# Performance work log

Hardware: AMD Instinct MI355X
Metric: run time of the kernel (lower is better)

## Reference

```python
import jax, jax.numpy as jnp
import numpy as np
from jax import lax

# Model hyperparameters (match init_kwargs)
DIM = 512
N_HEADS = 8
HEAD_DIM = DIM // N_HEADS
N_LAYERS = 4
N_LEVELS = 3          # len(chunk_sizes); CMS forward = stack of MLPs per level
HIDDEN = 4 * DIM
VOCAB = 50257
MAX_SEQ = 2048
B, S = 1, 2048
LN_EPS = 1e-5


def layer_norm(x, w, b):
    m = x.mean(-1, keepdims=True)
    v = ((x - m) ** 2).mean(-1, keepdims=True)
    return (x - m) * lax.rsqrt(v + LN_EPS) * w + b


def linear_attention(x, wq, wk, wv, wo):
    """LinearAttentionWithMemory: fast-weight recurrence M += k v^T, ksum += k,
    y_t = (M_t q_t) / (ksum_t . q_t + 1e-6). x: (B,S,DIM). Weights stored (in,out)."""
    Bn, Sn, D = x.shape
    fmap = lambda z: jax.nn.elu(z) + 1.0  # elu(x)+1 feature map
    # (B,S,D) -> (S,B,H,d) for scan over time
    def proj(w):
        return fmap(x @ w).reshape(Bn, Sn, N_HEADS, HEAD_DIM).transpose(1, 0, 2, 3)
    q = proj(wq)
    k = proj(wk)
    v = fmap(x @ wv).reshape(Bn, Sn, N_HEADS, HEAD_DIM).transpose(1, 0, 2, 3)
    # NOTE: original applies feature_map only to Q and K; V is raw projection
    v = (x @ wv).reshape(Bn, Sn, N_HEADS, HEAD_DIM).transpose(1, 0, 2, 3)

    def step(carry, inp):
        M, ksum = carry            # M: (B,H,d,d), ksum: (B,H,d)
        q_t, k_t, v_t = inp        # each (B,H,d)
        M = M + k_t[..., :, None] * v_t[..., None, :]
        ksum = ksum + k_t
        num = jnp.einsum('bhde,bhd->bhe', M, q_t)
        den = jnp.einsum('bhd,bhd->bh', ksum, q_t)[..., None] + 1e-6
        return (M, ksum), num / den

    carry0 = (jnp.zeros((Bn, N_HEADS, HEAD_DIM, HEAD_DIM), x.dtype),
              jnp.zeros((Bn, N_HEADS, HEAD_DIM), x.dtype))
    _, ys = lax.scan(step, carry0, (q, k, v))          # ys: (S,B,H,d)
    out = ys.transpose(1, 0, 2, 3).reshape(Bn, Sn, D)
    return out @ wo


def cms(x, w1, b1, w2, b2):
    """Continuum Memory System forward: sequential chain of per-level MLPs
    (chunk sizes only control parameter-update frequency during training).
    w1: (N_LEVELS, DIM, HIDDEN), w2: (N_LEVELS, HIDDEN, DIM)."""
    h = x
    for lvl in range(N_LEVELS):
        h = jax.nn.gelu(h @ w1[lvl] + b1[lvl]) @ w2[lvl] + b2[lvl]
    return h


def setup_inputs() -> dict:
    key = jax.random.key(0)
    ks = jax.random.split(key, 16)
    std = 0.02
    inp = {
        'tok_emb': jax.random.normal(ks[0], (VOCAB, DIM), jnp.float32) * std,
        'pos_emb': jax.random.normal(ks[1], (MAX_SEQ, DIM), jnp.float32) * std,
        'ln1_w': jnp.ones((N_LAYERS, DIM), jnp.float32),
        'ln1_b': jnp.zeros((N_LAYERS, DIM), jnp.float32),
        'wq': jax.random.normal(ks[2], (N_LAYERS, DIM, DIM), jnp.float32) * std,
        'wk': jax.random.normal(ks[3], (N_LAYERS, DIM, DIM), jnp.float32) * std,
        'wv': jax.random.normal(ks[4], (N_LAYERS, DIM, DIM), jnp.float32) * std,
        'wo': jax.random.normal(ks[5], (N_LAYERS, DIM, DIM), jnp.float32) * std,
        'ln2_w': jnp.ones((N_LAYERS, DIM), jnp.float32),
        'ln2_b': jnp.zeros((N_LAYERS, DIM), jnp.float32),
        'cms_w1': jax.random.normal(ks[6], (N_LAYERS, N_LEVELS, DIM, HIDDEN), jnp.float32) * std,
        'cms_b1': jnp.zeros((N_LAYERS, N_LEVELS, HIDDEN), jnp.float32),
        'cms_w2': jax.random.normal(ks[7], (N_LAYERS, N_LEVELS, HIDDEN, DIM), jnp.float32) * std,
        'cms_b2': jnp.zeros((N_LAYERS, N_LEVELS, DIM), jnp.float32),
        'lnf_w': jnp.ones((DIM,), jnp.float32),
        'lnf_b': jnp.zeros((DIM,), jnp.float32),
        'input_ids': jax.random.randint(ks[8], (B, S), 0, VOCAB, jnp.int32),
    }
    return inp


def reference(tok_emb, pos_emb, ln1_w, ln1_b, wq, wk, wv, wo,
              ln2_w, ln2_b, cms_w1, cms_b1, cms_w2, cms_b2,
              lnf_w, lnf_b, input_ids):
    seq_len = input_ids.shape[1]
    x = tok_emb[input_ids] + pos_emb[:seq_len][None, :, :]
    for l in range(N_LAYERS):
        x = x + linear_attention(layer_norm(x, ln1_w[l], ln1_b[l]),
                                 wq[l], wk[l], wv[l], wo[l])
        x = x + cms(layer_norm(x, ln2_w[l], ln2_b[l]),
                    cms_w1[l], cms_b1[l], cms_w2[l], cms_b2[l])
    x = layer_norm(x, lnf_w, lnf_b)
    logits = x @ tok_emb.T  # tied head weights
    return logits
```

## Files before the change

kernel.cpp:

```cpp
#include <hip/hip_runtime.h>

#define SQL 2048
#define DIM 512
#define NHEADS 8
#define HD 64
#define NLAYERS 4
#define NLEVELS 3
#define HID 2048
#define VOC 50257
#define CHUNK 64
#define NCHUNK 32
#define SD (SQL * DIM)
#define DD (DIM * DIM)

typedef __attribute__((ext_vector_type(8))) short bf16x8;
typedef __attribute__((ext_vector_type(4))) float f32x4;

__device__ __forceinline__ float gelu_f(float x) {
    float x3 = x * x * x;
    return 0.5f * x * (1.f + tanhf(0.7978845608028654f * (x + 0.044715f * x3)));
}
__device__ __forceinline__ float fmap_f(float x) {
    return x > 0.f ? x + 1.f : expf(x);
}
__device__ __forceinline__ unsigned short f2bf(float x) {
    unsigned int u = __float_as_uint(x);
    u = (u + 0x7fffu + ((u >> 16) & 1u)) >> 16;
    return (unsigned short)u;
}
__device__ __forceinline__ float bf2f(unsigned short h) {
    return __uint_as_float(((unsigned int)h) << 16);
}

__global__ __launch_bounds__(256) void embed_k(
    const float* __restrict__ tok, const float* __restrict__ pos,
    const int* __restrict__ ids, float* __restrict__ x)
{
    int idx = blockIdx.x * 256 + threadIdx.x;
    int t = idx >> 9;
    int d = idx & 511;
    x[idx] = tok[(size_t)ids[t] * DIM + d] + pos[idx];
}

__global__ __launch_bounds__(256) void ln_k(
    const float* __restrict__ in, unsigned short* __restrict__ oh,
    unsigned short* __restrict__ ol,
    const float* __restrict__ w, const float* __restrict__ b)
{
    int t = blockIdx.x, tid = threadIdx.x;
    float v0 = in[t * DIM + tid];
    float v1 = in[t * DIM + 256 + tid];
    float s = v0 + v1, sq = v0 * v0 + v1 * v1;
    #pragma unroll
    for (int off = 32; off > 0; off >>= 1) {
        s  += __shfl_down(s, off);
        sq += __shfl_down(sq, off);
    }
    __shared__ float ss[4], sqs[4];
    int wave = tid >> 6, lane = tid & 63;
    if (lane == 0) { ss[wave] = s; sqs[wave] = sq; }
    __syncthreads();
    float S  = ss[0] + ss[1] + ss[2] + ss[3];
    float SQ = sqs[0] + sqs[1] + sqs[2] + sqs[3];
    float m   = S * (1.f / DIM);
    float var = SQ * (1.f / DIM) - m * m;
    float rs  = rsqrtf(var + 1e-5f);
    float y0 = (v0 - m) * rs * w[tid]       + b[tid];
    float y1 = (v1 - m) * rs * w[256 + tid] + b[256 + tid];
    unsigned short h0 = f2bf(y0), h1 = f2bf(y1);
    oh[t * DIM + tid]       = h0;
    ol[t * DIM + tid]       = f2bf(y0 - bf2f(h0));
    oh[t * DIM + 256 + tid] = h1;
    ol[t * DIM + 256 + tid] = f2bf(y1 - bf2f(h1));
}

__global__ __launch_bounds__(256) void conv_rh_k(
    const float* __restrict__ in, unsigned short* __restrict__ oh, long long n4)
{
    long long i = (long long)blockIdx.x * 256 + threadIdx.x;
    if (i >= n4) return;
    float4 v = ((const float4*)in)[i];
    ushort4 hh;
    hh.x = f2bf(v.x); hh.y = f2bf(v.y); hh.z = f2bf(v.z); hh.w = f2bf(v.w);
    ((ushort4*)oh)[i] = hh;
}

__global__ __launch_bounds__(256) void conv_t_k(
    const float* __restrict__ in, unsigned short* __restrict__ oh,
    unsigned short* __restrict__ ol, int K, int N,
    size_t srcZ, size_t dstZ)
{
    in += (size_t)blockIdx.z * srcZ;
    oh += (size_t)blockIdx.z * dstZ;
    ol += (size_t)blockIdx.z * dstZ;
    __shared__ float T[32][33];
    const int n0 = blockIdx.x * 32, k0 = blockIdx.y * 32;
    const int tr = threadIdx.x >> 3, tc = threadIdx.x & 7;
    float4 v = *(const float4*)(in + (size_t)(k0 + tr) * N + n0 + tc * 4);
    T[tr][tc * 4 + 0] = v.x;
    T[tr][tc * 4 + 1] = v.y;
    T[tr][tc * 4 + 2] = v.z;
    T[tr][tc * 4 + 3] = v.w;
    __syncthreads();
    float o0 = T[tc * 4 + 0][tr];
    float o1 = T[tc * 4 + 1][tr];
    float o2 = T[tc * 4 + 2][tr];
    float o3 = T[tc * 4 + 3][tr];
    unsigned short h0 = f2bf(o0), h1 = f2bf(o1), h2 = f2bf(o2), h3 = f2bf(o3);
    ushort4 hh; hh.x = h0; hh.y = h1; hh.z = h2; hh.w = h3;
    ushort4 ll;
    ll.x = f2bf(o0 - bf2f(h0));
    ll.y = f2bf(o1 - bf2f(h1));
    ll.z = f2bf(o2 - bf2f(h2));
    ll.w = f2bf(o3 - bf2f(h3));
    size_t off = (size_t)(n0 + tr) * K + k0 + tc * 4;
    *(ushort4*)(oh + off) = hh;
    *(ushort4*)(ol + off) = ll;
}

template<int ACT, bool RES, bool PLANES, bool NG, bool X3, bool MSWAP, int BN>
__global__ __launch_bounds__(256) void gemm_t(
    const unsigned short* __restrict__ Ah, const unsigned short* __restrict__ Al,
    const unsigned short* __restrict__ Bh, const unsigned short* __restrict__ Bl,
    const float* __restrict__ bias, const float* __restrict__ Rsrc,
    float* __restrict__ C, unsigned short* __restrict__ Oh,
    unsigned short* __restrict__ Ol,
    int M, int N, int K, int fthr)
{
    constexpr int NW = BN / 2;
    constexpr int NF = NW / 16;
    __shared__ unsigned short sAh[4096], sAl[4096];
    __shared__ unsigned short sBh[BN * 32];
    __shared__ unsigned short sBl[X3 ? BN * 32 : 64];

    const int tid  = threadIdx.x;
    const int w    = tid >> 6, lane = tid & 63;
    const int r    = lane & 15, kq = lane >> 4;
    const int wr   = w >> 1, wc = w & 1;
    const int m0   = (MSWAP ? blockIdx.x : blockIdx.y) * 128;
    const int n0   = (MSWAP ? blockIdx.y : blockIdx.x) * BN;

    const int srow = tid >> 2;
    const int sch  = tid & 3;
    const int ar0 = m0 + srow, ar1 = ar0 + 64;
    int br0 = n0 + srow;
    if (NG) br0 = br0 < N ? br0 : N - 1;
    const unsigned short* pAh0 = Ah + (size_t)ar0 * K + sch * 8;
    const unsigned short* pAh1 = Ah + (size_t)ar1 * K + sch * 8;
    const unsigned short* pAl0 = Al + (size_t)ar0 * K + sch * 8;
    const unsigned short* pAl1 = Al + (size_t)ar1 * K + sch * 8;
    const unsigned short* pBh0 = Bh + (size_t)br0 * K + sch * 8;
    const unsigned short* pBl0 = X3 ? Bl + (size_t)br0 * K + sch * 8 : nullptr;
    const unsigned short* pBh1 = nullptr;
    const unsigned short* pBl1 = nullptr;
    if constexpr (BN == 128) {
        int br1 = n0 + 64 + srow;
        if (NG) br1 = br1 < N ? br1 : N - 1;
        pBh1 = Bh + (size_t)br1 * K + sch * 8;
        if constexpr (X3) pBl1 = Bl + (size_t)br1 * K + sch * 8;
    }

    bf16x8 rAh0 = *(const bf16x8*)pAh0, rAh1 = *(const bf16x8*)pAh1;
    bf16x8 rAl0 = *(const bf16x8*)pAl0, rAl1 = *(const bf16x8*)pAl1;
    bf16x8 rBh0 = *(const bf16x8*)pBh0;
    bf16x8 rBh1{}, rBl0{}, rBl1{};
    if constexpr (X3) rBl0 = *(const bf16x8*)pBl0;
    if constexpr (BN == 128) {
        rBh1 = *(const bf16x8*)pBh1;
        if constexpr (X3) rBl1 = *(const bf16x8*)pBl1;
    }

    f32x4 acc[4][NF] = {};
    const int sw = tid * 8;

    for (int ks = 0; ks < K; ks += 32) {
        __syncthreads();
        *(bf16x8*)&sAh[sw] = rAh0;  *(bf16x8*)&sAh[sw + 2048] = rAh1;
        *(bf16x8*)&sAl[sw] = rAl0;  *(bf16x8*)&sAl[sw + 2048] = rAl1;
        *(bf16x8*)&sBh[sw] = rBh0;
        if constexpr (BN == 128) *(bf16x8*)&sBh[sw + 2048] = rBh1;
        if constexpr (X3) {
            *(bf16x8*)&sBl[sw] = rBl0;
            if constexpr (BN == 128) *(bf16x8*)&sBl[sw + 2048] = rBl1;
        }
        __syncthreads();

        if (ks + 32 < K) {
            pAh0 += 32; pAh1 += 32; pAl0 += 32; pAl1 += 32;
            pBh0 += 32;
            rAh0 = *(const bf16x8*)pAh0; rAh1 = *(const bf16x8*)pAh1;
            rAl0 = *(const bf16x8*)pAl0; rAl1 = *(const bf16x8*)pAl1;
            rBh0 = *(const bf16x8*)pBh0;
            if constexpr (X3) { pBl0 += 32; rBl0 = *(const bf16x8*)pBl0; }
            if constexpr (BN == 128) {
                pBh1 += 32; rBh1 = *(const bf16x8*)pBh1;
                if constexpr (X3) { pBl1 += 32; rBl1 = *(const bf16x8*)pBl1; }
            }
        }

        bf16x8 a_h[4], a_l[4];
        #pragma unroll
        for (int mi = 0; mi < 4; ++mi) {
            const int off = (wr * 64 + mi * 16 + r) * 32 + kq * 8;
            a_h[mi] = *(const bf16x8*)&sAh[off];
            a_l[mi] = *(const bf16x8*)&sAl[off];
        }
        #pragma unroll
        for (int ni = 0; ni < NF; ++ni) {
            const int off = (wc * NW + ni * 16 + r) * 32 + kq * 8;
            const bf16x8 b_h = *(const bf16x8*)&sBh[off];
            #pragma unroll
            for (int mi = 0; mi < 4; ++mi) {
                acc[mi][ni] = __builtin_amdgcn_mfma_f32_16x16x32_bf16(
                    a_h[mi], b_h, acc[mi][ni], 0, 0, 0);
                acc[mi][ni] = __builtin_amdgcn_mfma_f32_16x16x32_bf16(
                    a_l[mi], b_h, acc[mi][ni], 0, 0, 0);
            }
            if constexpr (X3) {
                const bf16x8 b_l = *(const bf16x8*)&sBl[off];
                #pragma unroll
                for (int mi = 0; mi < 4; ++mi)
                    acc[mi][ni] = __builtin_amdgcn_mfma_f32_16x16x32_bf16(
                        a_h[mi], b_l, acc[mi][ni], 0, 0, 0);
            }
        }
    }

    #pragma unroll
    for (int mi = 0; mi < 4; ++mi)
        #pragma unroll
        for (int ni = 0; ni < NF; ++ni) {
            const int nn = n0 + wc * NW + ni * 16 + r;
            if (NG && nn >= N) continue;
            #pragma unroll
            for (int g = 0; g < 4; ++g) {
                const int mm = m0 + wr * 64 + mi * 16 + kq * 4 + g;
                float v = acc[mi][ni][g];
                if (bias) v += bias[nn];
                if (ACT == 2) v = gelu_f(v);
                if (ACT == 3) v = (nn < fthr) ? fmap_f(v) : v;
                const size_t o = (size_t)mm * N + nn;
                if (PLANES) {
                    unsigned short h = f2bf(v);
                    Oh[o] = h;
                    Ol[o] = f2bf(v - bf2f(h));
                } else {
                    if (RES) v += Rsrc[o];
                    C[o] = v;
                }
            }
        }
}

template<int ACT, bool RES, bool PLANES>
__global__ __launch_bounds__(512) void gemm_ks(
    const unsigned short* __restrict__ Ah, const unsigned short* __restrict__ Al,
    const unsigned short* __restrict__ Bh, const unsigned short* __restrict__ Bl,
    const float* __restrict__ bias, const float* __restrict__ Rsrc,
    float* __restrict__ C, unsigned short* __restrict__ Oh,
    unsigned short* __restrict__ Ol,
    int M, int N, int K, int fthr)
{
    const int tid  = threadIdx.x;
    const int w    = tid >> 6;
    const int lane = tid & 63;
    const int r  = lane & 15;
    const int kq = lane >> 4;
    const int m0 = blockIdx.y * 64, n0 = blockIdx.x * 64;
    const int Kw = K >> 3;

    f32x4 acc[4][4] = {};

    size_t aoff[4], boff[4];
    #pragma unroll
    for (int i = 0; i < 4; ++i) {
        aoff[i] = (size_t)(m0 + i * 16 + r) * K + w * Kw + kq * 8;
        boff[i] = (size_t)(n0 + i * 16 + r) * K + w * Kw + kq * 8;
    }

    for (int k0 = 0; k0 < Kw; k0 += 32) {
        bf16x8 ah[4], al4[4], bh[4], bl4[4];
        #pragma unroll
        for (int i = 0; i < 4; ++i) {
            ah[i]  = *(const bf16x8*)(Ah + aoff[i] + k0);
            al4[i] = *(const bf16x8*)(Al + aoff[i] + k0);
            bh[i]  = *(const bf16x8*)(Bh + boff[i] + k0);
            bl4[i] = *(const bf16x8*)(Bl + boff[i] + k0);
        }
        #pragma unroll
        for (int mi = 0; mi < 4; ++mi)
            #pragma unroll
            for (int ni = 0; ni < 4; ++ni) {
                acc[mi][ni] = __builtin_amdgcn_mfma_f32_16x16x32_bf16(
                    ah[mi], bh[ni], acc[mi][ni], 0, 0, 0);
                acc[mi][ni] = __builtin_amdgcn_mfma_f32_16x16x32_bf16(
                    ah[mi], bl4[ni], acc[mi][ni], 0, 0, 0);
                acc[mi][ni] = __builtin_amdgcn_mfma_f32_16x16x32_bf16(
                    al4[mi], bh[ni], acc[mi][ni], 0, 0, 0);
            }
    }

    __shared__ f32x4 red[8][64][8];

    #pragma unroll
    for (int R = 0; R < 2; ++R) {
        if (R) __syncthreads();
        #pragma unroll
        for (int mh = 0; mh < 2; ++mh) {
            const int mi = R * 2 + mh;
            const int q2 = mh * 4 + kq;
            #pragma unroll
            for (int ni = 0; ni < 4; ++ni) {
                const int cc = ni * 16 + r;
                red[w][cc][q2 ^ (cc & 7)] = acc[mi][ni];
            }
        }
        __syncthreads();
        const int col = tid & 63;
        const int q2  = tid >> 6;
        const int swz = q2 ^ (col & 7);
        f32x4 s = red[0][col][swz];
        #pragma unroll
        for (int ww = 1; ww < 8; ++ww) s += red[ww][col][swz];
        const int gn = n0 + col;
        float bv = bias ? bias[gn] : 0.f;
        #pragma unroll
        for (int e = 0; e < 4; ++e) {
            const int gm = m0 + R * 32 + q2 * 4 + e;
            float v = s[e] + bv;
            if (ACT == 2) v = gelu_f(v);
            if (ACT == 3) v = (gn < fthr) ? fmap_f(v) : v;
            const size_t o = (size_t)gm * N + gn;
            if (PLANES) {
                unsigned short h = f2bf(v);
                Oh[o] = h;
                Ol[o] = f2bf(v - bf2f(h));
            } else {
                if (RES) v += Rsrc[o];
                C[o] = v;
            }
        }
    }
}

__global__ __launch_bounds__(256) void attn_p1(
    const float* __restrict__ kbuf, const float* __restrict__ vbuf,
    float* __restrict__ Mc, float* __restrict__ ksum, int rs)
{
    const int h = blockIdx.x >> 5, c = blockIdx.x & 31;
    const int tid = threadIdx.x;
    const int tx = tid & 15, ty = tid >> 4;
    __shared__ float Ks[CHUNK][HD + 1];
    __shared__ float Vs[CHUNK][HD + 1];
    #pragma unroll
    for (int i = 0; i < 16; ++i) {
        int idx = tid + i * 256;
        int t = idx >> 6, d = idx & 63;
        size_t g = (size_t)(c * CHUNK + t) * rs + h * HD + d;
        Ks[t][d] = kbuf[g];
        Vs[t][d] = vbuf[g];
    }
    __syncthreads();

    float acc[4][4] = {};
    for (int t = 0; t < CHUNK; ++t) {
        float ka[4], vb[4];
        #pragma unroll
        for (int i = 0; i < 4; ++i) ka[i] = Ks[t][ty * 4 + i];
        #pragma unroll
        for (int j = 0; j < 4; ++j) vb[j] = Vs[t][tx * 4 + j];
        #pragma unroll
        for (int i = 0; i < 4; ++i)
            #pragma unroll
            for (int j = 0; j < 4; ++j)
                acc[i][j] += ka[i] * vb[j];
    }
    const size_t base = (size_t)(h * NCHUNK + c) * HD * HD;
    #pragma unroll
    for (int i = 0; i < 4; ++i)
        #pragma unroll
        for (int j = 0; j < 4; ++j)
            Mc[base + (size_t)(ty * 4 + i) * HD + tx * 4 + j] = acc[i][j];

    if (tid < HD) {
        float s = 0.f;
        for (int t = 0; t < CHUNK; ++t) s += Ks[t][tid];
        ksum[(size_t)(h * NCHUNK + c) * HD + tid] = s;
    }
}

__global__ __launch_bounds__(64) void attn_scan(
    float* __restrict__ Mc, float* __restrict__ ksum)
{
    const int b = blockIdx.x;
    const int h = b / 65, p = b % 65;
    const int tid = threadIdx.x;
    float v[NCHUNK];
    if (p < HD) {
        const size_t base = ((size_t)(h * NCHUNK) * HD + p) * HD + tid;
        #pragma unroll
        for (int c = 0; c < NCHUNK; ++c)
            v[c] = Mc[base + (size_t)c * HD * HD];
        float run = 0.f;
        #pragma unroll
        for (int c = 0; c < NCHUNK; ++c) {
            Mc[base + (size_t)c * HD * HD] = run;
            run += v[c];
        }
    } else {
        const size_t base = (size_t)(h * NCHUNK) * HD + tid;
        #pragma unroll
        for (int c = 0; c < NCHUNK; ++c)
            v[c] = ksum[base + (size_t)c * HD];
        float run = 0.f;
        #pragma unroll
        for (int c = 0; c < NCHUNK; ++c) {
            ksum[base + (size_t)c * HD] = run;
            run += v[c];
        }
    }
}

__global__ __launch_bounds__(256) void attn_p3(
    const float* __restrict__ qbuf, const float* __restrict__ kbuf,
    const float* __restrict__ vbuf, const float* __restrict__ Mc,
    const float* __restrict__ ksum,
    unsigned short* __restrict__ aoh, unsigned short* __restrict__ aol, int rs)
{
    const int h = blockIdx.x >> 5, c = blockIdx.x & 31;
    const int tid = threadIdx.x;
    const int tx = tid & 15, ty = tid >> 4;
    __shared__ float Qs[CHUNK][HD + 1];
    __shared__ float Ks[CHUNK][HD + 1];
    __shared__ float Vs[CHUNK][HD + 1];
    __shared__ float Ss[CHUNK][CHUNK + 1];
    __shared__ float Ms[HD][HD + 1];
    __shared__ float kp[HD], den[CHUNK];

    const size_t mbase = (size_t)(h * NCHUNK + c) * HD * HD;
    #pragma unroll
    for (int i = 0; i < 16; ++i) {
        int idx = tid + i * 256;
        int t = idx >> 6, d = idx & 63;
        size_t g = (size_t)(c * CHUNK + t) * rs + h * HD + d;
        Qs[t][d] = qbuf[g];
        Ks[t][d] = kbuf[g];
        Vs[t][d] = vbuf[g];
        Ms[t][d] = Mc[mbase + (size_t)t * HD + d];
    }
    if (tid < HD) kp[tid] = ksum[(size_t)(h * NCHUNK + c) * HD + tid];
    __syncthreads();

    {
        float acc[4][4] = {};
        for (int d = 0; d < HD; ++d) {
            float qa[4], kb[4];
            #pragma unroll
            for (int i = 0; i < 4; ++i) qa[i] = Qs[ty * 4 + i][d];
            #pragma unroll
            for (int j = 0; j < 4; ++j) kb[j] = Ks[tx * 4 + j][d];
            #pragma unroll
            for (int i = 0; i < 4; ++i)
                #pragma unroll
                for (int j = 0; j < 4; ++j)
                    acc[i][j] += qa[i] * kb[j];
        }
        #pragma unroll
        for (int i = 0; i < 4; ++i)
            #pragma unroll
            for (int j = 0; j < 4; ++j) {
                int t = ty * 4 + i, u = tx * 4 + j;
                Ss[t][u] = (u <= t) ? acc[i][j] : 0.f;
            }
    }
    __syncthreads();

    if (tid < CHUNK) {
        int t = tid;
        float s = 1e-6f;
        for (int d = 0; d < HD; ++d) s += Qs[t][d] * kp[d];
        for (int u = 0; u < CHUNK; ++u) s += Ss[t][u];
        den[t] = s;
    }
    __syncthreads();

    {
        float acc[4][4] = {};
        for (int d = 0; d < HD; ++d) {
            float qa[4], mb[4];
            #pragma unroll
            for (int i = 0; i < 4; ++i) qa[i] = Qs[ty * 4 + i][d];
            #pragma unroll
            for (int j = 0; j < 4; ++j) mb[j] = Ms[d][tx * 4 + j];
            #pragma unroll
            for (int i = 0; i < 4; ++i)
                #pragma unroll
                for (int j = 0; j < 4; ++j)
                    acc[i][j] += qa[i] * mb[j];
        }
        for (int u = 0; u < CHUNK; ++u) {
            float sa[4], vb[4];
            #pragma unroll
            for (int i = 0; i < 4; ++i) sa[i] = Ss[ty * 4 + i][u];
            #pragma unroll
            for (int j = 0; j < 4; ++j) vb[j] = Vs[u][tx * 4 + j];
            #pragma unroll
            for (int i = 0; i < 4; ++i)
                #pragma unroll
                for (int j = 0; j < 4; ++j)
                    acc[i][j] += sa[i] * vb[j];
        }
        #pragma unroll
        for (int i = 0; i < 4; ++i) {
            int t = ty * 4 + i;
            float inv = 1.f / den[t];
            #pragma unroll
            for (int j = 0; j < 4; ++j) {
                float vv = acc[i][j] * inv;
                unsigned short hh = f2bf(vv);
                size_t o = (size_t)(c * CHUNK + t) * DIM + h * HD + tx * 4 + j;
                aoh[o] = hh;
                aol[o] = f2bf(vv - bf2f(hh));
            }
        }
    }
}

extern "C" void kernel_launch(void* const* d_in, const int* in_sizes, int n_in,
                              void* d_out, int out_size, void* d_ws, size_t ws_size,
                              hipStream_t stream)
{
    const float* tok  = (const float*)d_in[0];
    const float* pos  = (const float*)d_in[1];
    const float* ln1w = (const float*)d_in[2];
    const float* ln1b = (const float*)d_in[3];
    const float* wq   = (const float*)d_in[4];
    const float* wk   = (const float*)d_in[5];
    const float* wv   = (const float*)d_in[6];
    const float* wo   = (const float*)d_in[7];
    const float* ln2w = (const float*)d_in[8];
    const float* ln2b = (const float*)d_in[9];
    const float* w1   = (const float*)d_in[10];
    const float* b1   = (const float*)d_in[11];
    const float* w2   = (const float*)d_in[12];
    const float* b2   = (const float*)d_in[13];
    const float* lnfw = (const float*)d_in[14];
    const float* lnfb = (const float*)d_in[15];
    const int*   ids  = (const int*)d_in[16];
    float* outp = (float*)d_out;

    typedef unsigned short us;
    char* p = (char*)d_ws;
    float* x   = (float*)p; p += (size_t)SD * 4;
    float* qkv = (float*)p; p += (size_t)SQL * 3 * DIM * 4;
    float* Mc  = (float*)p; p += (size_t)NHEADS * NCHUNK * HD * HD * 4;
    float* ksm = (float*)p; p += (size_t)NHEADS * NCHUNK * HD * 4;

    us* xnH = (us*)p; p += (size_t)SD * 2;
    us* xnL = (us*)p; p += (size_t)SD * 2;
    us* aoH = (us*)p; p += (size_t)SD * 2;
    us* aoL = (us*)p; p += (size_t)SD * 2;
    us* cinH = (us*)p; p += (size_t)SD * 2;
    us* cinL = (us*)p; p += (size_t)SD * 2;
    us* h1H = (us*)p; p += (size_t)SQL * HID * 2;
    us* h1L = (us*)p; p += (size_t)SQL * HID * 2;
    us* tokH = (us*)p; p += (size_t)VOC * DIM * 2;
    us* wqkvH = (us*)p; p += (size_t)NLAYERS * 3 * DD * 2;
    us* wqkvL = (us*)p; p += (size_t)NLAYERS * 3 * DD * 2;
    us* woH = (us*)p; p += (size_t)NLAYERS * DD * 2;
    us* woL = (us*)p; p += (size_t)NLAYERS * DD * 2;
    const size_t W1SZ = (size_t)NLAYERS * NLEVELS * DIM * HID;
    us* w1H = (us*)p; p += W1SZ * 2;
    us* w1L = (us*)p; p += W1SZ * 2;
    us* w2H = (us*)p; p += W1SZ * 2;
    us* w2L = (us*)p; p += W1SZ * 2;

    {
        long long n4 = (long long)VOC * DIM / 4;
        conv_rh_k<<<(unsigned)((n4 + 255) / 256), 256, 0, stream>>>(tok, tokH, n4);
        dim3 gt(DIM / 32, DIM / 32, NLAYERS);
        conv_t_k<<<gt, 256, 0, stream>>>(wq, wqkvH,          wqkvL,          DIM, DIM, DD, (size_t)3 * DD);
        conv_t_k<<<gt, 256, 0, stream>>>(wk, wqkvH + DD,     wqkvL + DD,     DIM, DIM, DD, (size_t)3 * DD);
        conv_t_k<<<gt, 256, 0, stream>>>(wv, wqkvH + 2 * DD, wqkvL + 2 * DD, DIM, DIM, DD, (size_t)3 * DD);
        conv_t_k<<<gt, 256, 0, stream>>>(wo, woH, woL, DIM, DIM, DD, DD);
        dim3 g1(HID / 32, DIM / 32, NLAYERS * NLEVELS);
        conv_t_k<<<g1, 256, 0, stream>>>(w1, w1H, w1L, DIM, HID,
                                         (size_t)DIM * HID, (size_t)DIM * HID);
        dim3 g2(DIM / 32, HID / 32, NLAYERS * NLEVELS);
        conv_t_k<<<g2, 256, 0, stream>>>(w2, w2H, w2L, HID, DIM,
                                         (size_t)DIM * HID, (size_t)DIM * HID);
    }

    embed_k<<<SD / 256, 256, 0, stream>>>(tok, pos, ids, x);

    const dim3 gqkv(3 * DIM / 64, SQL / 128);
    const dim3 g512(DIM / 64, SQL / 64);
    const dim3 gw1(HID / 64, SQL / 128);
    const dim3 ghead(SQL / 128, (VOC + 127) / 128);
    const int RS = 3 * DIM;

    for (int l = 0; l < NLAYERS; ++l) {
        ln_k<<<SQL, 256, 0, stream>>>(x, xnH, xnL, ln1w + l * DIM, ln1b + l * DIM);
        gemm_t<3, false, false, false, true, false, 64><<<gqkv, 256, 0, stream>>>(
            xnH, xnL, wqkvH + (size_t)l * 3 * DD, wqkvL + (size_t)l * 3 * DD,
            nullptr, nullptr, qkv, nullptr, nullptr, SQL, 3 * DIM, DIM, 2 * DIM);
        attn_p1<<<NHEADS * NCHUNK, 256, 0, stream>>>(qkv + DIM, qkv + 2 * DIM, Mc, ksm, RS);
        attn_scan<<<NHEADS * 65, 64, 0, stream>>>(Mc, ksm);
        attn_p3<<<NHEADS * NCHUNK, 256, 0, stream>>>(
            qkv, qkv + DIM, qkv + 2 * DIM, Mc, ksm, aoH, aoL, RS);
        gemm_ks<0, true, false><<<g512, 512, 0, stream>>>(
            aoH, aoL, woH + (size_t)l * DD, woL + (size_t)l * DD,
            nullptr, x, x, nullptr, nullptr, SQL, DIM, DIM, 0);

        ln_k<<<SQL, 256, 0, stream>>>(x, xnH, xnL, ln2w + l * DIM, ln2b + l * DIM);
        const us* cH = xnH; const us* cL = xnL;
        for (int lvl = 0; lvl < NLEVELS; ++lvl) {
            const size_t off1 = (size_t)(l * NLEVELS + lvl) * DIM * HID;
            const float* b1p = b1 + (size_t)(l * NLEVELS + lvl) * HID;
            const float* b2p = b2 + (size_t)(l * NLEVELS + lvl) * DIM;
            gemm_t<2, false, true, false, true, false, 64><<<gw1, 256, 0, stream>>>(
                cH, cL, w1H + off1, w1L + off1, b1p, nullptr,
                nullptr, h1H, h1L, SQL, HID, DIM, 0);
            if (lvl < NLEVELS - 1) {
                gemm_ks<0, false, true><<<g512, 512, 0, stream>>>(
                    h1H, h1L, w2H + off1, w2L + off1, b2p, nullptr,
                    nullptr, cinH, cinL, SQL, DIM, HID, 0);
                cH = cinH; cL = cinL;
            } else {
                gemm_ks<0, true, false><<<g512, 512, 0, stream>>>(
                    h1H, h1L, w2H + off1, w2L + off1, b2p, x,
                    x, nullptr, nullptr, SQL, DIM, HID, 0);
            }
        }
    }

    ln_k<<<SQL, 256, 0, stream>>>(x, xnH, xnL, lnfw, lnfb);
    gemm_t<0, false, false, true, false, true, 128><<<ghead, 256, 0, stream>>>(
        xnH, xnL, tokH, nullptr, nullptr, nullptr,
        outp, nullptr, nullptr, SQL, VOC, DIM, 0);
}
```

Baseline: 1.844 ms.

## Fuse layernorm into QKV and CMS-W1 GEMM prologue; widen LM head tile

Removes the separate ln_k launches before the QKV projection and the first CMS level. The GEMM now computes per-row mean and rstd from the fp32 residual and normalises and splits A into hi/lo bf16 planes while loading. The B-tile loading is generalised to BN/64 slices, and the tied-head GEMM moves from BN=128 to BN=256 tiles. The fused prologue recomputes the normalisation in every N-tile block, repeating it across many blocks. The larger head tile raises register and LDS use and may lower occupancy.

```diff
diff --git a/kernel.cpp b/kernel.cpp
--- a/kernel.cpp
+++ b/kernel.cpp
@@ -118,20 +118,25 @@
     *(ushort4*)(ol + off) = ll;
 }
 
-template<int ACT, bool RES, bool PLANES, bool NG, bool X3, bool MSWAP, int BN>
+template<int ACT, bool RES, bool PLANES, bool NG, bool X3, bool MSWAP, int BN, bool LNP>
 __global__ __launch_bounds__(256) void gemm_t(
     const unsigned short* __restrict__ Ah, const unsigned short* __restrict__ Al,
+    const float* __restrict__ Ax, const float* __restrict__ lnw,
+    const float* __restrict__ lnb,
     const unsigned short* __restrict__ Bh, const unsigned short* __restrict__ Bl,
     const float* __restrict__ bias, const float* __restrict__ Rsrc,
     float* __restrict__ C, unsigned short* __restrict__ Oh,
     unsigned short* __restrict__ Ol,
     int M, int N, int K, int fthr)
 {
+    constexpr int NS = BN / 64;
     constexpr int NW = BN / 2;
     constexpr int NF = NW / 16;
     __shared__ unsigned short sAh[4096], sAl[4096];
     __shared__ unsigned short sBh[BN * 32];
     __shared__ unsigned short sBl[X3 ? BN * 32 : 64];
+    __shared__ float sMean[LNP ? 128 : 1], sRstd[LNP ? 128 : 1];
+    __shared__ float sW[LNP ? 512 : 1], sB2[LNP ? 512 : 1];
 
     const int tid  = threadIdx.x;
     const int w    = tid >> 6, lane = tid & 63;
@@ -143,32 +148,83 @@
     const int srow = tid >> 2;
     const int sch  = tid & 3;
     const int ar0 = m0 + srow, ar1 = ar0 + 64;
-    int br0 = n0 + srow;
-    if (NG) br0 = br0 < N ? br0 : N - 1;
-    const unsigned short* pAh0 = Ah + (size_t)ar0 * K + sch * 8;
-    const unsigned short* pAh1 = Ah + (size_t)ar1 * K + sch * 8;
-    const unsigned short* pAl0 = Al + (size_t)ar0 * K + sch * 8;
-    const unsigned short* pAl1 = Al + (size_t)ar1 * K + sch * 8;
-    const unsigned short* pBh0 = Bh + (size_t)br0 * K + sch * 8;
-    const unsigned short* pBl0 = X3 ? Bl + (size_t)br0 * K + sch * 8 : nullptr;
-    const unsigned short* pBh1 = nullptr;
-    const unsigned short* pBl1 = nullptr;
-    if constexpr (BN == 128) {
-        int br1 = n0 + 64 + srow;
-        if (NG) br1 = br1 < N ? br1 : N - 1;
-        pBh1 = Bh + (size_t)br1 * K + sch * 8;
-        if constexpr (X3) pBl1 = Bl + (size_t)br1 * K + sch * 8;
-    }
-
-    bf16x8 rAh0 = *(const bf16x8*)pAh0, rAh1 = *(const bf16x8*)pAh1;
-    bf16x8 rAl0 = *(const bf16x8*)pAl0, rAl1 = *(const bf16x8*)pAl1;
-    bf16x8 rBh0 = *(const bf16x8*)pBh0;
-    bf16x8 rBh1{}, rBl0{}, rBl1{};
-    if constexpr (X3) rBl0 = *(const bf16x8*)pBl0;
-    if constexpr (BN == 128) {
-        rBh1 = *(const bf16x8*)pBh1;
-        if constexpr (X3) rBl1 = *(const bf16x8*)pBl1;
-    }
+
+    if constexpr (LNP) {
+        __shared__ float pS[256], pQ[256];
+        const int r2 = tid >> 1, hf = tid & 1;
+        const float* rp = Ax + (size_t)(m0 + r2) * 512 + hf * 256;
+        float s = 0.f, q = 0.f;
+        for (int i = 0; i < 64; ++i) {
+            float4 v = ((const float4*)rp)[i];
+            s += v.x + v.y + v.z + v.w;
+            q += v.x * v.x + v.y * v.y + v.z * v.z + v.w * v.w;
+        }
+        pS[tid] = s; pQ[tid] = q;
+        sW[tid]  = lnw[tid]; sW[256 + tid]  = lnw[256 + tid];
+        sB2[tid] = lnb[tid]; sB2[256 + tid] = lnb[256 + tid];
+        __syncthreads();
+        if (hf == 0) {
+            float S = s + pS[tid + 1], Q = q + pQ[tid + 1];
+            float m  = S * (1.f / 512.f);
+            float var = Q * (1.f / 512.f) - m * m;
+            sMean[r2] = m;
+            sRstd[r2] = rsqrtf(var + 1e-5f);
+        }
+        __syncthreads();
+    }
+
+    const unsigned short* pB[NS];
+    const unsigned short* pBlo[X3 ? NS : 1];
+    #pragma unroll
+    for (int s2 = 0; s2 < NS; ++s2) {
+        int br = n0 + s2 * 64 + srow;
+        if (NG) br = br < N ? br : N - 1;
+        pB[s2] = Bh + (size_t)br * K + sch * 8;
+        if constexpr (X3) pBlo[s2] = Bl + (size_t)br * K + sch * 8;
+    }
+
+    bf16x8 rAh0, rAh1, rAl0, rAl1;
+    bf16x8 rB[NS];
+    bf16x8 rBlo[X3 ? NS : 1];
+
+    auto loadA = [&](int kk) {
+        if constexpr (LNP) {
+            #pragma unroll
+            for (int hh = 0; hh < 2; ++hh) {
+                const int rr = hh ? ar1 : ar0;
+                const float mn = sMean[srow + hh * 64];
+                const float rs = sRstd[srow + hh * 64];
+                const float* pp = Ax + (size_t)rr * 512 + kk + sch * 8;
+                float4 u0 = *(const float4*)pp;
+                float4 u1 = *(const float4*)(pp + 4);
+                float ys[8] = {u0.x, u0.y, u0.z, u0.w, u1.x, u1.y, u1.z, u1.w};
+                bf16x8 hv, lv;
+                #pragma unroll
+                for (int j = 0; j < 8; ++j) {
+                    const int ci = kk + sch * 8 + j;
+                    float y = (ys[j] - mn) * rs * sW[ci] + sB2[ci];
+                    unsigned short hb = f2bf(y);
+                    hv[j] = (short)hb;
+                    lv[j] = (short)f2bf(y - bf2f(hb));
+                }
+                if (hh) { rAh1 = hv; rAl1 = lv; } else { rAh0 = hv; rAl0 = lv; }
+            }
+        } else {
+            rAh0 = *(const bf16x8*)(Ah + (size_t)ar0 * K + kk + sch * 8);
+            rAh1 = *(const bf16x8*)(Ah + (size_t)ar1 * K + kk + sch * 8);
+            rAl0 = *(const bf16x8*)(Al + (size_t)ar0 * K + kk + sch * 8);
+            rAl1 = *(const bf16x8*)(Al + (size_t)ar1 * K + kk + sch * 8);
+        }
+    };
+    auto loadB = [&](int kk) {
+        #pragma unroll
+        for (int s2 = 0; s2 < NS; ++s2) {
+            rB[s2] = *(const bf16x8*)(pB[s2] + kk);
+            if constexpr (X3) rBlo[s2] = *(const bf16x8*)(pBlo[s2] + kk);
+        }
+    };
+
+    loadA(0); loadB(0);
 
     f32x4 acc[4][NF] = {};
     const int sw = tid * 8;
@@ -177,25 +233,16 @@
         __syncthreads();
         *(bf16x8*)&sAh[sw] = rAh0;  *(bf16x8*)&sAh[sw + 2048] = rAh1;
         *(bf16x8*)&sAl[sw] = rAl0;  *(bf16x8*)&sAl[sw + 2048] = rAl1;
-        *(bf16x8*)&sBh[sw] = rBh0;
-        if constexpr (BN == 128) *(bf16x8*)&sBh[sw + 2048] = rBh1;
-        if constexpr (X3) {
-            *(bf16x8*)&sBl[sw] = rBl0;
-            if constexpr (BN == 128) *(bf16x8*)&sBl[sw + 2048] = rBl1;
+        #pragma unroll
+        for (int s2 = 0; s2 < NS; ++s2) {
+            *(bf16x8*)&sBh[sw + s2 * 2048] = rB[s2];
+            if constexpr (X3) *(bf16x8*)&sBl[sw + s2 * 2048] = rBlo[s2];
         }
         __syncthreads();
 
         if (ks + 32 < K) {
-            pAh0 += 32; pAh1 += 32; pAl0 += 32; pAl1 += 32;
-            pBh0 += 32;
-            rAh0 = *(const bf16x8*)pAh0; rAh1 = *(const bf16x8*)pAh1;
-            rAl0 = *(const bf16x8*)pAl0; rAl1 = *(const bf16x8*)pAl1;
-            rBh0 = *(const bf16x8*)pBh0;
-            if constexpr (X3) { pBl0 += 32; rBl0 = *(const bf16x8*)pBl0; }
-            if constexpr (BN == 128) {
-                pBh1 += 32; rBh1 = *(const bf16x8*)pBh1;
-                if constexpr (X3) { pBl1 += 32; rBl1 = *(const bf16x8*)pBl1; }
-            }
+            loadA(ks + 32);
+            loadB(ks + 32);
         }
 
         bf16x8 a_h[4], a_l[4];
@@ -596,13 +643,13 @@
     const dim3 gqkv(3 * DIM / 64, SQL / 128);
     const dim3 g512(DIM / 64, SQL / 64);
     const dim3 gw1(HID / 64, SQL / 128);
-    const dim3 ghead(SQL / 128, (VOC + 127) / 128);
+    const dim3 ghead(SQL / 128, (VOC + 255) / 256);
     const int RS = 3 * DIM;
 
     for (int l = 0; l < NLAYERS; ++l) {
-        ln_k<<<SQL, 256, 0, stream>>>(x, xnH, xnL, ln1w + l * DIM, ln1b + l * DIM);
-        gemm_t<3, false, false, false, true, false, 64><<<gqkv, 256, 0, stream>>>(
-            xnH, xnL, wqkvH + (size_t)l * 3 * DD, wqkvL + (size_t)l * 3 * DD,
+        gemm_t<3, false, false, false, true, false, 64, true><<<gqkv, 256, 0, stream>>>(
+            nullptr, nullptr, x, ln1w + l * DIM, ln1b + l * DIM,
+            wqkvH + (size_t)l * 3 * DD, wqkvL + (size_t)l * 3 * DD,
             nullptr, nullptr, qkv, nullptr, nullptr, SQL, 3 * DIM, DIM, 2 * DIM);
         attn_p1<<<NHEADS * NCHUNK, 256, 0, stream>>>(qkv + DIM, qkv + 2 * DIM, Mc, ksm, RS);
         attn_scan<<<NHEADS * 65, 64, 0, stream>>>(Mc, ksm);
@@ -612,20 +659,25 @@
             aoH, aoL, woH + (size_t)l * DD, woL + (size_t)l * DD,
             nullptr, x, x, nullptr, nullptr, SQL, DIM, DIM, 0);
 
-        ln_k<<<SQL, 256, 0, stream>>>(x, xnH, xnL, ln2w + l * DIM, ln2b + l * DIM);
-        const us* cH = xnH; const us* cL = xnL;
         for (int lvl = 0; lvl < NLEVELS; ++lvl) {
             const size_t off1 = (size_t)(l * NLEVELS + lvl) * DIM * HID;
             const float* b1p = b1 + (size_t)(l * NLEVELS + lvl) * HID;
             const float* b2p = b2 + (size_t)(l * NLEVELS + lvl) * DIM;
-            gemm_t<2, false, true, false, true, false, 64><<<gw1, 256, 0, stream>>>(
-                cH, cL, w1H + off1, w1L + off1, b1p, nullptr,
-                nullptr, h1H, h1L, SQL, HID, DIM, 0);
+            if (lvl == 0) {
+                gemm_t<2, false, true, false, true, false, 64, true><<<gw1, 256, 0, stream>>>(
+                    nullptr, nullptr, x, ln2w + l * DIM, ln2b + l * DIM,
+                    w1H + off1, w1L + off1, b1p, nullptr,
+                    nullptr, h1H, h1L, SQL, HID, DIM, 0);
+            } else {
+                gemm_t<2, false, true, false, true, false, 64, false><<<gw1, 256, 0, stream>>>(
+                    cinH, cinL, nullptr, nullptr, nullptr,
+                    w1H + off1, w1L + off1, b1p, nullptr,
+                    nullptr, h1H, h1L, SQL, HID, DIM, 0);
+            }
             if (lvl < NLEVELS - 1) {
                 gemm_ks<0, false, true><<<g512, 512, 0, stream>>>(
                     h1H, h1L, w2H + off1, w2L + off1, b2p, nullptr,
                     nullptr, cinH, cinL, SQL, DIM, HID, 0);
-                cH = cinH; cL = cinL;
             } else {
                 gemm_ks<0, true, false><<<g512, 512, 0, stream>>>(
                     h1H, h1L, w2H + off1, w2L + off1, b2p, x,
@@ -635,7 +687,8 @@
     }
 
     ln_k<<<SQL, 256, 0, stream>>>(x, xnH, xnL, lnfw, lnfb);
-    gemm_t<0, false, false, true, false, true, 128><<<ghead, 256, 0, stream>>>(
-        xnH, xnL, tokH, nullptr, nullptr, nullptr,
+    gemm_t<0, false, false, true, false, true, 256, false><<<ghead, 256, 0, stream>>>(
+        xnH, xnL, nullptr, nullptr, nullptr,
+        tokH, nullptr, nullptr, nullptr,
         outp, nullptr, nullptr, SQL, VOC, DIM, 0);
 }
```

Measured after the change: 2.042 ms. +10.7%, slower.
